# Kernel tuning notes

Measured on AMD Instinct MI355X. Metric: run time of the kernel, lower is better.

## Reference

```python
import jax, jax.numpy as jnp
import numpy as np

GROUPS = 32
EPS = 1e-5


def setup_inputs() -> dict:
    key = jax.random.key(0)
    ks = jax.random.split(key, 6)
    B, H, W, C = 2, 64, 64, 512
    wscale = 0.02  # keep logits in a sane range for softmax
    return {
        "x": jax.random.normal(ks[0], (B, H, W, C), dtype=jnp.float32),
        "gamma": jnp.ones((C,), jnp.float32),
        "beta": jnp.zeros((C,), jnp.float32),
        "wq": jax.random.normal(ks[1], (C, C), dtype=jnp.float32) * wscale,
        "bq": jnp.zeros((C,), jnp.float32),
        "wk": jax.random.normal(ks[2], (C, C), dtype=jnp.float32) * wscale,
        "bk": jnp.zeros((C,), jnp.float32),
        "wv": jax.random.normal(ks[3], (C, C), dtype=jnp.float32) * wscale,
        "bv": jnp.zeros((C,), jnp.float32),
        "wp": jax.random.normal(ks[4], (C, C), dtype=jnp.float32) * wscale,
        "bp": jnp.zeros((C,), jnp.float32),
    }


def _group_norm(x, gamma, beta):
    B, H, W, C = x.shape
    xg = x.reshape(B, H, W, GROUPS, C // GROUPS)
    mean = xg.mean(axis=(1, 2, 4), keepdims=True)
    var = xg.var(axis=(1, 2, 4), keepdims=True)
    xn = ((xg - mean) * jax.lax.rsqrt(var + EPS)).reshape(B, H, W, C)
    return xn * gamma + beta


def reference(x, gamma, beta, wq, bq, wk, bk, wv, bv, wp, bp):
    B, H, W, C = x.shape
    xn = _group_norm(x, gamma, beta)
    # 1x1 convs == per-pixel linear layers
    q = (xn @ wq + bq).reshape(B, H * W, C)
    k = (xn @ wk + bk).reshape(B, H * W, C)
    v = (xn @ wv + bv).reshape(B, H * W, C)
    scale = C ** (-0.5)
    attn = jax.nn.softmax(jnp.einsum("bqc,bkc->bqk", q, k) * scale, axis=-1)
    out = jnp.einsum("bqk,bkc->bqc", attn, v).reshape(B, H, W, C)
    return (out @ wp + bp) + x
```

## Files before the change

kernel.cpp:

```cpp
#include <hip/hip_runtime.h>


typedef __bf16 bf16_t;
typedef __bf16 bf16x8 __attribute__((ext_vector_type(8)));
typedef __bf16 bf16x4 __attribute__((ext_vector_type(4)));
typedef float  f32x4  __attribute__((ext_vector_type(4)));

__device__ __forceinline__ bf16x8 ld8(const bf16_t* p) {
    return *reinterpret_cast<const bf16x8*>(p);
}
__device__ __forceinline__ f32x4 mfma16(bf16x8 a, bf16x8 b, f32x4 c) {
    return __builtin_amdgcn_mfma_f32_16x16x32_bf16(a, b, c, 0, 0, 0);
}
__device__ __forceinline__ void gload16(const bf16_t* gp, bf16_t* lp) {
    __builtin_amdgcn_global_load_lds(
        (const __attribute__((address_space(1))) void*)gp,
        (__attribute__((address_space(3))) void*)lp, 16, 0, 0);
}

#define NPIX 8192
#define C512 512
#define SEQ  4096
#define QSCALE 0.044194173824159216f

__global__ __launch_bounds__(256) void gn_sum_k(const float* __restrict__ x,
                                                float* __restrict__ accum) {
    int bg    = blockIdx.x >> 3;
    int slice = blockIdx.x & 7;
    int b = bg >> 5, g = bg & 31;
    const float* xp = x + (size_t)b * SEQ * C512 + g * 16;
    float s = 0.f, s2 = 0.f;
    #pragma unroll
    for (int pp = 0; pp < 2; pp++) {
        int p = slice * 512 + pp * 256 + threadIdx.x;
        const float4* q = reinterpret_cast<const float4*>(xp + (size_t)p * C512);
        #pragma unroll
        for (int i = 0; i < 4; i++) {
            float4 v = q[i];
            s  += v.x + v.y + v.z + v.w;
            s2 += v.x*v.x + v.y*v.y + v.z*v.z + v.w*v.w;
        }
    }
    #pragma unroll
    for (int off = 32; off >= 1; off >>= 1) {
        s  += __shfl_down(s, off);
        s2 += __shfl_down(s2, off);
    }
    __shared__ float rs[4], rs2[4];
    int wave = threadIdx.x >> 6;
    if ((threadIdx.x & 63) == 0) { rs[wave] = s; rs2[wave] = s2; }
    __syncthreads();
    if (threadIdx.x == 0) {
        float S = rs[0] + rs[1] + rs[2] + rs[3];
        float S2 = rs2[0] + rs2[1] + rs2[2] + rs2[3];
        atomicAdd(&accum[bg * 2],     S);
        atomicAdd(&accum[bg * 2 + 1], S2);
    }
}

__global__ __launch_bounds__(256) void wt_conv_k(const float* wq, const float* wk,
                                                 const float* wv, const float* wp,
                                                 const float* bq, const float* bk,
                                                 const float* bv,
                                                 bf16_t* wqkvT, bf16_t* wpT,
                                                 float* bqkv) {
    int y = blockIdx.y;
    if (y == 4) {
        if (blockIdx.x >= 6) return;
        int i = blockIdx.x * 256 + threadIdx.x;
        float v = (i < 512) ? bq[i] * QSCALE : (i < 1024) ? bk[i - 512] : bv[i - 1024];
        bqkv[i] = v;
        return;
    }
    const float* w = (y == 0) ? wq : (y == 1) ? wk : (y == 2) ? wv : wp;
    float scale = (y == 0) ? QSCALE : 1.0f;
    int tid = blockIdx.x * 256 + threadIdx.x;
    int n = tid >> 9, k = tid & 511;
    bf16_t val = (bf16_t)(w[(size_t)k * C512 + n] * scale);
    if (y < 3) wqkvT[((size_t)y * C512 + n) * C512 + k] = val;
    else       wpT[(size_t)n * C512 + k] = val;
}

__global__ __launch_bounds__(256) void xn_k(const float* __restrict__ x,
                                            const float* __restrict__ accum,
                                            const float* __restrict__ gamma,
                                            const float* __restrict__ beta,
                                            bf16_t* __restrict__ xn) {
    size_t idx = ((size_t)blockIdx.x * 256 + threadIdx.x) * 4;
    int c = (int)(idx & 511);
    size_t pix = idx >> 9;
    int b = (int)(pix >> 12);
    int g = c >> 4;
    float sum = accum[(b * 32 + g) * 2];
    float ssq = accum[(b * 32 + g) * 2 + 1];
    float mean = sum * (1.f / 65536.f);
    float var  = ssq * (1.f / 65536.f) - mean * mean;
    float rstd = rsqrtf(var + 1e-5f);
    float4 v  = *reinterpret_cast<const float4*>(x + idx);
    float4 gm = *reinterpret_cast<const float4*>(gamma + c);
    float4 bt = *reinterpret_cast<const float4*>(beta + c);
    bf16x4 o;
    o[0] = (bf16_t)((v.x - mean) * rstd * gm.x + bt.x);
    o[1] = (bf16_t)((v.y - mean) * rstd * gm.y + bt.y);
    o[2] = (bf16_t)((v.z - mean) * rstd * gm.z + bt.z);
    o[3] = (bf16_t)((v.w - mean) * rstd * gm.w + bt.w);
    *reinterpret_cast<bf16x4*>(xn + idx) = o;
}

template <int MODE>
__global__ __launch_bounds__(256, 2) void gemm128_k(
        const bf16_t* __restrict__ Aall, const bf16_t* __restrict__ Ball,
        const float* __restrict__ bias, const float* __restrict__ resid,
        void* __restrict__ out0, void* __restrict__ out1,
        void* __restrict__ out2, void* __restrict__ out3,
        float* __restrict__ lsum) {
    constexpr int TM  = (MODE == 3) ? 64 : 128;
    constexpr int ASZ = TM * 32;
    constexpr int ACH = TM / 16;
    constexpr int CPW = (ACH + 8) / 4;
    constexpr int MI  = TM / 32;
    __shared__ bf16_t smem[2 * ASZ + 8192];

    int lane = threadIdx.x & 63;
    int w    = threadIdx.x >> 6;
    int wr   = w >> 1, wc = w & 1;
    int lrow = lane & 15, quad = lane >> 4;

    const bf16_t* A  = Aall;
    const bf16_t* A1 = (MODE == 3) ? (const bf16_t*)out1 : nullptr;
    const bf16_t* B  = Ball;
    size_t lda = 512, ldb = 512;
    int ksteps = (MODE == 3) ? 32 : 16;

    int bm = blockIdx.x * TM, bn = blockIdx.y * 128;

    auto stage = [&](int buf, int ks) {
        const bf16_t* Ap = (MODE == 3 && ks >= 16) ? A1 : A;
        size_t k0 = (size_t)(MODE == 3 ? (ks & 15) : ks) * 32;
        #pragma unroll
        for (int ii = 0; ii < CPW; ii++) {
            int c = w * CPW + ii;
            if (c < ACH) {
                const bf16_t* gpA = Ap + (size_t)(bm + c * 16 + lrow) * lda + k0 + quad * 8;
                gload16(gpA, &smem[buf * ASZ + c * 512]);
            } else {
                int cb = c - ACH;
                const bf16_t* gpB = B + (size_t)(bn + cb * 16 + lrow) * ldb + k0 + quad * 8;
                gload16(gpB, &smem[2 * ASZ + buf * 4096 + cb * 512]);
            }
        }
    };

    f32x4 acc[MI][4] = {};

    stage(0, 0);

    for (int ks = 0; ks < ksteps; ks++) {
        int cur = ks & 1;
        __syncthreads();
        if (ks + 1 < ksteps) stage(1 - cur, ks + 1);

        const bf16_t* al = &smem[cur * ASZ + (wr * MI) * 512];
        const bf16_t* bl = &smem[2 * ASZ + cur * 4096 + (wc * 4) * 512];
        bf16x8 af[MI], bf[4];
        #pragma unroll
        for (int m = 0; m < MI; m++) af[m] = ld8(al + m * 512 + lane * 8);
        #pragma unroll
        for (int n = 0; n < 4; n++) bf[n] = ld8(bl + n * 512 + lane * 8);
        #pragma unroll
        for (int m = 0; m < MI; m++)
            #pragma unroll
            for (int n = 0; n < 4; n++)
                acc[m][n] = mfma16(af[m], bf[n], acc[m][n]);
    }

    #pragma unroll
    for (int m = 0; m < MI; m++) {
        int rowb = bm + wr * (TM / 2) + m * 16 + quad * 4;
        #pragma unroll
        for (int n = 0; n < 4; n++) {
            int col = bn + wc * 64 + n * 16 + lrow;
            #pragma unroll
            for (int i = 0; i < 4; i++) {
                int row = rowb + i;
                float v = acc[m][n][i];
                if (MODE == 0) {
                    int seg = col >> 9, c = col & 511;
                    bf16_t val = (bf16_t)(v + bias[col]);
                    if (seg == 0) {
                        ((bf16_t*)out0)[(size_t)row * C512 + c] = val;
                    } else if (seg == 1) {
                        ((bf16_t*)out1)[(size_t)row * C512 + c] = val;
                    } else {
                        int b = row >> 12, s = row & 4095;
                        ((bf16_t*)out2)[((size_t)(b * C512 + c)) * SEQ + s] = val;
                    }
                } else {
                    size_t idx = (size_t)row * C512 + col;
                    float inv = 1.0f / lsum[row];
                    ((float*)out0)[idx] = v * inv + bias[col] + resid[idx];
                }
            }
        }
    }
}

__global__ __launch_bounds__(512, 1) void fattn_k(
        const bf16_t* __restrict__ Q, const bf16_t* __restrict__ K,
        const bf16_t* __restrict__ VT, bf16_t* __restrict__ Op0,
        bf16_t* __restrict__ Op1, float* __restrict__ lsum) {
    __shared__ bf16_t Kl[2][32 * 512];
    __shared__ bf16_t Vl[2][512 * 32];
    __shared__ bf16_t Pl[64 * 32];

    int bid = blockIdx.x;
    int xcd = bid & 7, loc = bid >> 3;
    int b   = (xcd >> 1) & 1;
    int kv  = xcd & 1;
    int q0  = ((xcd >> 2) * 32 + loc) * 64;
    int key0 = kv * 2048;

    const bf16_t* Qb = Q  + (size_t)b * SEQ * C512;
    const bf16_t* Kb = K  + (size_t)b * SEQ * C512;
    const bf16_t* Vb = VT + (size_t)b * C512 * SEQ;
    bf16_t* Op = kv ? Op1 : Op0;

    int lane = threadIdx.x & 63;
    int w    = threadIdx.x >> 6;
    int lrow = lane & 15, quad = lane >> 4;
    int qt = w & 3, kt = w >> 2;

    bf16x8 qf[16];
    const bf16_t* qp = Qb + (size_t)(q0 + qt * 16 + lrow) * C512 + quad * 8;
    #pragma unroll
    for (int ks = 0; ks < 16; ks++) qf[ks] = ld8(qp + ks * 32);

    auto stage = [&](int buf, int t) {
        #pragma unroll
        for (int ii = 0; ii < 8; ii++) {
            int cc = w * 8 + ii;
            if (cc < 32) {
                int ks = cc >> 1, ktc = cc & 1;
                const bf16_t* gp = Kb +
                    (size_t)(key0 + t * 32 + ktc * 16 + lrow) * C512 + ks * 32 + quad * 8;
                gload16(gp, &Kl[buf][cc * 512]);
            } else {
                int ct = cc - 32;
                const bf16_t* gp = Vb +
                    (size_t)(ct * 16 + lrow) * SEQ + key0 + t * 32 + quad * 8;
                gload16(gp, &Vl[buf][ct * 512]);
            }
        }
    };

    f32x4 oacc[4][4] = {};
    float rs[4] = {0.f, 0.f, 0.f, 0.f};

    stage(0, 0);

    for (int t = 0; t < 64; t++) {
        int cur = t & 1;
        __syncthreads();
        if (t < 63) stage(1 - cur, t + 1);

        f32x4 sa0 = {}, sa1 = {};
        __builtin_amdgcn_s_setprio(1);
        #pragma unroll
        for (int ks = 0; ks < 8; ks++) {
            bf16x8 kf0 = ld8(&Kl[cur][((2 * ks) * 2 + kt) * 512 + lane * 8]);
            bf16x8 kf1 = ld8(&Kl[cur][((2 * ks + 1) * 2 + kt) * 512 + lane * 8]);
            sa0 = mfma16(qf[2 * ks],     kf0, sa0);
            sa1 = mfma16(qf[2 * ks + 1], kf1, sa1);
        }
        __builtin_amdgcn_s_setprio(0);
        f32x4 sa = sa0 + sa1;
        #pragma unroll
        for (int i = 0; i < 4; i++) {
            float p = __expf(fminf(sa[i], 20.0f));
            rs[i] += p;
            int off = qt * 512 + (quad * 4 + i) * 8 +
                      (kt * 2 + (lrow >> 3)) * 128 + (lrow & 7);
            Pl[off] = (bf16_t)p;
        }
        asm volatile("s_waitcnt lgkmcnt(0)" ::: "memory");
        __builtin_amdgcn_s_barrier();
        __builtin_amdgcn_sched_barrier(0);

        bf16x8 pa[4];
        #pragma unroll
        for (int m = 0; m < 4; m++) pa[m] = ld8(&Pl[m * 512 + lane * 8]);
        __builtin_amdgcn_s_setprio(1);
        #pragma unroll
        for (int n = 0; n < 4; n++) {
            bf16x8 vf = ld8(&Vl[cur][(w * 4 + n) * 512 + lane * 8]);
            #pragma unroll
            for (int m = 0; m < 4; m++)
                oacc[m][n] = mfma16(pa[m], vf, oacc[m][n]);
        }
        __builtin_amdgcn_s_setprio(0);
    }

    #pragma unroll
    for (int i = 0; i < 4; i++) {
        float r = rs[i];
        r += __shfl_xor(r, 1);
        r += __shfl_xor(r, 2);
        r += __shfl_xor(r, 4);
        r += __shfl_xor(r, 8);
        if (lrow == 0)
            atomicAdd(&lsum[(size_t)b * SEQ + q0 + qt * 16 + quad * 4 + i], r);
    }

    #pragma unroll
    for (int m = 0; m < 4; m++) {
        int row = q0 + m * 16 + quad * 4;
        #pragma unroll
        for (int n = 0; n < 4; n++) {
            int col = w * 64 + n * 16 + lrow;
            #pragma unroll
            for (int i = 0; i < 4; i++)
                Op[((size_t)b * SEQ + row + i) * C512 + col] = (bf16_t)oacc[m][n][i];
        }
    }
}

extern "C" void kernel_launch(void* const* d_in, const int* in_sizes, int n_in,
                              void* d_out, int out_size, void* d_ws, size_t ws_size,
                              hipStream_t stream) {
    const float* x     = (const float*)d_in[0];
    const float* gamma = (const float*)d_in[1];
    const float* beta  = (const float*)d_in[2];
    const float* wq = (const float*)d_in[3];  const float* bq = (const float*)d_in[4];
    const float* wk = (const float*)d_in[5];  const float* bk = (const float*)d_in[6];
    const float* wv = (const float*)d_in[7];  const float* bv = (const float*)d_in[8];
    const float* wp = (const float*)d_in[9];  const float* bp = (const float*)d_in[10];
    float* out = (float*)d_out;

    char* ws = (char*)d_ws;
    size_t off = 0;
    float*  bqkv   = (float*)(ws + off);   off += 1536 * sizeof(float);
    float*  lsum   = (float*)(ws + off);   off += (size_t)NPIX * sizeof(float);
    float*  accum  = (float*)(ws + off);   off += 128 * sizeof(float);
    bf16_t* xn     = (bf16_t*)(ws + off);  off += (size_t)NPIX * C512 * 2;
    bf16_t* wqkvT  = (bf16_t*)(ws + off);  off += (size_t)3 * C512 * C512 * 2;
    bf16_t* wpT    = (bf16_t*)(ws + off);  off += (size_t)C512 * C512 * 2;
    bf16_t* Qb     = (bf16_t*)(ws + off);  off += (size_t)NPIX * C512 * 2;
    bf16_t* Kb     = (bf16_t*)(ws + off);  off += (size_t)NPIX * C512 * 2;
    bf16_t* VTb    = (bf16_t*)(ws + off);  off += (size_t)NPIX * C512 * 2;
    bf16_t* Op0    = (bf16_t*)(ws + off);  off += (size_t)NPIX * C512 * 2;
    bf16_t* Op1    = (bf16_t*)(ws + off);  off += (size_t)NPIX * C512 * 2;

    hipMemsetAsync(lsum, 0, (size_t)(NPIX + 128) * sizeof(float), stream);

    gn_sum_k<<<512, 256, 0, stream>>>(x, accum);
    wt_conv_k<<<dim3(1024, 5), 256, 0, stream>>>(wq, wk, wv, wp, bq, bk, bv,
                                                 wqkvT, wpT, bqkv);
    xn_k<<<4096, 256, 0, stream>>>(x, accum, gamma, beta, xn);

    gemm128_k<0><<<dim3(64, 12, 1), 256, 0, stream>>>(
        xn, wqkvT, bqkv, nullptr, Qb, Kb, VTb, nullptr, nullptr);

    fattn_k<<<256, 512, 0, stream>>>(Qb, Kb, VTb, Op0, Op1, lsum);

    gemm128_k<3><<<dim3(128, 4, 1), 256, 0, stream>>>(
        Op0, wpT, bp, x, out, Op1, nullptr, nullptr, lsum);
}
```

Measured before the change: 304.5 us.

## Transpose V through LDS for coalesced stores; simplify QK MFMA chain

In the QKV projection GEMM, the tile that produces V is now staged in shared memory and written out transposed with 16-byte vector stores. This replaces the scattered 2-byte strided global writes into the V^T layout. The shared buffer grows to a padded 128x136 tile for this mode, which may lower occupancy. The attention kernel also goes back to a single serial MFMA accumulator chain for QK^T and drops the s_setprio hints, which lengthens the dependency chain.

```diff
diff --git a/kernel.cpp b/kernel.cpp
--- a/kernel.cpp
+++ b/kernel.cpp
@@ -119,7 +119,8 @@
     constexpr int ACH = TM / 16;
     constexpr int CPW = (ACH + 8) / 4;
     constexpr int MI  = TM / 32;
-    __shared__ bf16_t smem[2 * ASZ + 8192];
+    constexpr int SME = (MODE == 0) ? (128 * 136) : (2 * ASZ + 8192);
+    __shared__ bf16_t smem[SME];
 
     int lane = threadIdx.x & 63;
     int w    = threadIdx.x >> 6;
@@ -174,6 +175,35 @@
                 acc[m][n] = mfma16(af[m], bf[n], acc[m][n]);
     }
 
+    if (MODE == 0 && bn >= 1024) {
+        __syncthreads();
+        #pragma unroll
+        for (int m = 0; m < MI; m++) {
+            int lr0 = wr * 64 + m * 16 + quad * 4;
+            #pragma unroll
+            for (int n = 0; n < 4; n++) {
+                int lc = wc * 64 + n * 16 + lrow;
+                float bsc = bias[bn + lc];
+                #pragma unroll
+                for (int i = 0; i < 4; i++)
+                    smem[(lr0 + i) * 136 + lc] = (bf16_t)(acc[m][n][i] + bsc);
+            }
+        }
+        __syncthreads();
+        int cc = threadIdx.x >> 1, sh = threadIdx.x & 1;
+        int b = bm >> 12, s0 = (bm & 4095) + sh * 64;
+        bf16_t* VTp = (bf16_t*)out2 +
+                      ((size_t)(b * C512 + (bn - 1024) + cc)) * SEQ + s0;
+        #pragma unroll
+        for (int j = 0; j < 8; j++) {
+            bf16x8 v;
+            #pragma unroll
+            for (int e = 0; e < 8; e++)
+                v[e] = smem[(sh * 64 + j * 8 + e) * 136 + cc];
+            *reinterpret_cast<bf16x8*>(VTp + j * 8) = v;
+        }
+        return;
+    }
     #pragma unroll
     for (int m = 0; m < MI; m++) {
         int rowb = bm + wr * (TM / 2) + m * 16 + quad * 4;
@@ -187,14 +217,8 @@
                 if (MODE == 0) {
                     int seg = col >> 9, c = col & 511;
                     bf16_t val = (bf16_t)(v + bias[col]);
-                    if (seg == 0) {
-                        ((bf16_t*)out0)[(size_t)row * C512 + c] = val;
-                    } else if (seg == 1) {
-                        ((bf16_t*)out1)[(size_t)row * C512 + c] = val;
-                    } else {
-                        int b = row >> 12, s = row & 4095;
-                        ((bf16_t*)out2)[((size_t)(b * C512 + c)) * SEQ + s] = val;
-                    }
+                    if (seg == 0) ((bf16_t*)out0)[(size_t)row * C512 + c] = val;
+                    else          ((bf16_t*)out1)[(size_t)row * C512 + c] = val;
                 } else {
                     size_t idx = (size_t)row * C512 + col;
                     float inv = 1.0f / lsum[row];
@@ -263,17 +287,12 @@
         __syncthreads();
         if (t < 63) stage(1 - cur, t + 1);
 
-        f32x4 sa0 = {}, sa1 = {};
-        __builtin_amdgcn_s_setprio(1);
-        #pragma unroll
-        for (int ks = 0; ks < 8; ks++) {
-            bf16x8 kf0 = ld8(&Kl[cur][((2 * ks) * 2 + kt) * 512 + lane * 8]);
-            bf16x8 kf1 = ld8(&Kl[cur][((2 * ks + 1) * 2 + kt) * 512 + lane * 8]);
-            sa0 = mfma16(qf[2 * ks],     kf0, sa0);
-            sa1 = mfma16(qf[2 * ks + 1], kf1, sa1);
-        }
-        __builtin_amdgcn_s_setprio(0);
-        f32x4 sa = sa0 + sa1;
+        f32x4 sa = {0.f, 0.f, 0.f, 0.f};
+        #pragma unroll
+        for (int ks = 0; ks < 16; ks++) {
+            bf16x8 bf = ld8(&Kl[cur][(ks * 2 + kt) * 512 + lane * 8]);
+            sa = mfma16(qf[ks], bf, sa);
+        }
         #pragma unroll
         for (int i = 0; i < 4; i++) {
             float p = __expf(fminf(sa[i], 20.0f));
@@ -289,7 +308,6 @@
         bf16x8 pa[4];
         #pragma unroll
         for (int m = 0; m < 4; m++) pa[m] = ld8(&Pl[m * 512 + lane * 8]);
-        __builtin_amdgcn_s_setprio(1);
         #pragma unroll
         for (int n = 0; n < 4; n++) {
             bf16x8 vf = ld8(&Vl[cur][(w * 4 + n) * 512 + lane * 8]);
@@ -297,7 +315,6 @@
             for (int m = 0; m < 4; m++)
                 oacc[m][n] = mfma16(pa[m], vf, oacc[m][n]);
         }
-        __builtin_amdgcn_s_setprio(0);
     }
 
     #pragma unroll
```

Measured after the change: 303.0 us, median of 2. No clear change (-0.5%).
